# Performance work log

Measured on AMD Instinct MI355X. Metric: run time of the kernel, lower is better.

The kernel has to match this reference:

```python
import jax, jax.numpy as jnp
import numpy as np

B, N, DIN, D, L = 16, 256, 32, 64, 3  # batch, nodes, input feat, emb_dim, num_layer


def setup_inputs() -> dict:
    key = jax.random.key(0)
    ks = jax.random.split(key, 8)
    fea = jax.random.normal(ks[0], (B, N, DIN), jnp.float32)
    # binary dense adjacency (float, as the repo differentiates through it)
    adj = (jax.random.uniform(ks[1], (B, N, N)) < 0.125).astype(jnp.float32)

    def g(k, shape, scale=0.05):
        return jax.random.normal(k, shape, jnp.float32) * scale

    return dict(
        fea=fea, adj=adj,
        enc_W=g(ks[2], (DIN, D)), enc_b=jnp.zeros((D,), jnp.float32),
        bond_W=g(ks[3], (L, D)),            # Linear(1, D, bias=False) per layer
        eps=jnp.zeros((L,), jnp.float32),   # GIN eps per layer
        W1=g(ks[4], (L, D, 2 * D)), b1=jnp.zeros((L, 2 * D), jnp.float32),
        g1=jnp.ones((L, 2 * D), jnp.float32), be1=jnp.zeros((L, 2 * D), jnp.float32),
        W2=g(ks[5], (L, 2 * D, D)), b2=jnp.zeros((L, D), jnp.float32),
        gbn=jnp.ones((L, D), jnp.float32), bbn=jnp.zeros((L, D), jnp.float32),
    )


def _bn(x, gamma, beta, eps=1e-5):
    # BatchNorm1d in training mode: per-channel stats over (batch, nodes)
    m = x.mean((0, 1), keepdims=True)
    v = x.var((0, 1), keepdims=True)
    return (x - m) * jax.lax.rsqrt(v + eps) * gamma + beta


def reference(fea, adj, enc_W, enc_b, bond_W, eps, W1, b1, g1, be1, W2, b2, gbn, bbn):
    x = fea @ enc_W + enc_b                      # [B,N,D] atom_encoder
    adj_ones = jnp.where(adj > 1.0, 1.0, adj)    # clamp multi-bonds to 1
    for l in range(L):
        # GINConv: dense propagate -> message relu(x_j + edge_attr) -> sum over neighbors
        edge = adj[..., None] * bond_W[l]                    # bond_encoder: [B,N,N,D]
        x_j = adj_ones[..., None] * x[:, None, :, :]         # [B,N,N,D] broadcast gather
        agg = jax.nn.relu(x_j + edge).sum(-2)                # [B,N,D] sum-reduce
        h = (1.0 + eps[l]) * x + agg
        # mlp: Linear(D,2D) -> BN -> ReLU -> Linear(2D,D)
        h = _bn(h @ W1[l] + b1[l], g1[l], be1[l])
        h = jax.nn.relu(h) @ W2[l] + b2[l]
        # outer batch norm; ReLU except last layer (drop_ratio=0 -> dropout no-op)
        h = _bn(h, gbn[l], bbn[l])
        x = h if l == L - 1 else jax.nn.relu(h)
    return x  # JK='last'
```

## Files before the change

### kernel.cpp

```cpp
#include <hip/hip_runtime.h>

#define NN 256
#define DIN 32
#define DD 64
#define D2 128
#define RTOT 4096
#define GBD 256
#define RPB 16
#define GBC 512
#define RPC 8
#define AST 32

typedef float f32x4 __attribute__((ext_vector_type(4)));
typedef float f32x2 __attribute__((ext_vector_type(2)));

__device__ __forceinline__ void fma4(f32x4& o, float s, const f32x4 w) {
  o[0] = fmaf(s, w[0], o[0]); o[1] = fmaf(s, w[1], o[1]);
  o[2] = fmaf(s, w[2], o[2]); o[3] = fmaf(s, w[3], o[3]);
}

__global__ __launch_bounds__(256) void enc_kernel(
    const float* __restrict__ fea, const float* __restrict__ W,
    const float* __restrict__ bias, float* __restrict__ x,
    float* __restrict__ accz) {
  if (blockIdx.x < 48) {
#pragma unroll
    for (int i = 0; i < 4; ++i)
      accz[blockIdx.x * 1024 + i * 256 + threadIdx.x] = 0.f;
  }
  int g = blockIdx.x * 256 + threadIdx.x;
  int r = g >> 6, c = g & 63;
  const float* fr = fea + r * DIN;
  float acc = bias[c];
#pragma unroll
  for (int k = 0; k < DIN; ++k) acc = fmaf(fr[k], W[k * DD + c], acc);
  x[g] = acc;
}

__global__ __launch_bounds__(256) void bc_kernel(
    const float* __restrict__ adj, const float* __restrict__ x,
    const float* __restrict__ bondW, const float* __restrict__ epsp,
    const float* __restrict__ W1, const float* __restrict__ b1,
    const float* __restrict__ gbnp, const float* __restrict__ bbnp,
    const float* __restrict__ acc2p,
    int apply_bn,
    float* __restrict__ h1, float* __restrict__ acc1) {
  __shared__ float sY[NN * DD];
  __shared__ float sh[RPC * DD];
  __shared__ float sSB[2 * DD];
  __shared__ float pst[2 * RPC * D2];
  const int tid = threadIdx.x, bid = blockIdx.x;
  const int lane = tid & 63, wv = tid >> 6;
  const int b = bid >> 5;
  const int r0 = (bid & 31) * RPC;

  if (apply_bn && tid < DD) {
    float s = acc2p[tid * AST], q = acc2p[(64 + tid) * AST];
    float mean = s * (1.f / RTOT);
    float var = fmaf(-mean, mean, q * (1.f / RTOT));
    float sc = gbnp[tid] * rsqrtf(var + 1e-5f);
    sSB[tid] = sc;
    sSB[64 + tid] = fmaf(-mean, sc, bbnp[tid]);
  }
  __syncthreads();

  const float* xb = x + (size_t)b * NN * DD;

  float a[2][4];
#pragma unroll
  for (int rr = 0; rr < 2; ++rr) {
    const float* adjr = adj + ((size_t)b * NN + r0 + wv * 2 + rr) * NN + lane;
#pragma unroll
    for (int ck = 0; ck < 4; ++ck) a[rr][ck] = adjr[ck * 64];
  }
  float xo[2];
#pragma unroll
  for (int rr = 0; rr < 2; ++rr)
    xo[rr] = xb[(size_t)(r0 + wv * 2 + rr) * DD + lane];
  f32x4 yv[16];
  {
    const f32x4* xb4 = (const f32x4*)xb;
#pragma unroll
    for (int k = 0; k < 16; ++k) yv[k] = xb4[tid + k * 256];
  }

  unsigned long long m[2][4];
#pragma unroll
  for (int rr = 0; rr < 2; ++rr)
#pragma unroll
    for (int ck = 0; ck < 4; ++ck) m[rr][ck] = __ballot(a[rr][ck] != 0.f);

  {
    const int d0 = (tid & 15) * 4;
    f32x4 bw4 = *(const f32x4*)&bondW[d0];
    f32x4 aS = {0, 0, 0, 0}, aB = {0, 0, 0, 0};
    if (apply_bn) { aS = *(const f32x4*)&sSB[d0]; aB = *(const f32x4*)&sSB[64 + d0]; }
    f32x4* sy4 = (f32x4*)sY;
#pragma unroll
    for (int k = 0; k < 16; ++k) {
      f32x4 v = yv[k];
#pragma unroll
      for (int e = 0; e < 4; ++e) {
        float t = v[e];
        if (apply_bn) t = fmaxf(fmaf(t, aS[e], aB[e]), 0.f);
        v[e] = fmaxf(t + bw4[e], 0.f);
      }
      sy4[tid + k * 256] = v;
    }
  }
  __syncthreads();

  float S = 0.f, Bv = 0.f;
  if (apply_bn) { S = sSB[lane]; Bv = sSB[64 + lane]; }
  float epv = 1.f + epsp[0];
#pragma unroll
  for (int rr = 0; rr < 2; ++rr) {
    float av = 0.f;
#pragma unroll
    for (int ck = 0; ck < 4; ++ck) {
      unsigned long long mm = m[rr][ck];
      const float* yb = sY + ck * 64 * DD + lane;
      while (mm) {
        float v[8]; bool hb[8];
#pragma unroll
        for (int u = 0; u < 8; ++u) {
          bool ok = mm != 0ull;
          int j = ok ? (int)__builtin_ctzll(mm) : 0;
          mm &= mm - 1;
          hb[u] = ok;
          v[u] = yb[j * DD];
        }
#pragma unroll
        for (int u = 0; u < 8; ++u) av += hb[u] ? v[u] : 0.f;
      }
    }
    float xv = xo[rr];
    if (apply_bn) xv = fmaxf(fmaf(xv, S, Bv), 0.f);
    sh[(wv * 2 + rr) * DD + lane] = fmaf(epv, xv, av);
  }
  __syncthreads();

  {
    int row = tid >> 5, c0 = (tid & 31) * 4;
    f32x4 o = *(const f32x4*)&b1[c0];
#pragma unroll 4
    for (int d = 0; d < DD; d += 4) {
      f32x4 hv = *(const f32x4*)&sh[row * DD + d];
      f32x4 w0 = *(const f32x4*)&W1[(d + 0) * D2 + c0];
      f32x4 w1 = *(const f32x4*)&W1[(d + 1) * D2 + c0];
      f32x4 w2 = *(const f32x4*)&W1[(d + 2) * D2 + c0];
      f32x4 w3 = *(const f32x4*)&W1[(d + 3) * D2 + c0];
      fma4(o, hv[0], w0); fma4(o, hv[1], w1); fma4(o, hv[2], w2); fma4(o, hv[3], w3);
    }
    *(f32x4*)&h1[(size_t)(b * NN + r0 + row) * D2 + c0] = o;
    *(f32x4*)&pst[row * D2 + c0] = o;
    *(f32x4*)&pst[RPC * D2 + row * D2 + c0] = o * o;
  }
  __syncthreads();
  if (tid < D2) {
    float s = 0.f, q = 0.f;
#pragma unroll
    for (int g = 0; g < RPC; ++g) {
      s += pst[g * D2 + tid];
      q += pst[RPC * D2 + g * D2 + tid];
    }
    atomicAdd(acc1 + tid * AST, s);
    atomicAdd(acc1 + (128 + tid) * AST, q);
  }
}

__global__ __launch_bounds__(256) void d_kernel(
    const float* __restrict__ h1, const float* __restrict__ W2,
    const float* __restrict__ b2, const float* __restrict__ g1,
    const float* __restrict__ be1, float* __restrict__ h2,
    const float* __restrict__ acc1,
    float* __restrict__ acc2) {
  __shared__ float sW2[D2 * DD];
  __shared__ float sh1[RPB][D2 + 4];
  __shared__ float sS[D2], sB[D2];
  __shared__ float pst[2 * 8 * DD];
  int tid = threadIdx.x, bid = blockIdx.x;

  {
    const f32x4* w4 = (const f32x4*)W2;
    f32x4* s4 = (f32x4*)sW2;
#pragma unroll
    for (int i = 0; i < 8; ++i) s4[tid + i * 256] = w4[tid + i * 256];
  }
  if (tid < D2) {
    float mean = acc1[tid * AST] * (1.f / RTOT);
    float var = fmaf(-mean, mean, acc1[(128 + tid) * AST] * (1.f / RTOT));
    float sc = g1[tid] * rsqrtf(var + 1e-5f);
    sS[tid] = sc;
    sB[tid] = fmaf(-mean, sc, be1[tid]);
  }
  __syncthreads();
  {
    const f32x4* h14 = (const f32x4*)(h1 + (size_t)bid * RPB * D2);
#pragma unroll
    for (int ii = 0; ii < 2; ++ii) {
      int i = tid + ii * 256;
      f32x4 v = h14[i];
      int lr = i >> 5, c = (i & 31) * 4;
      v[0] = fmaxf(fmaf(v[0], sS[c + 0], sB[c + 0]), 0.f);
      v[1] = fmaxf(fmaf(v[1], sS[c + 1], sB[c + 1]), 0.f);
      v[2] = fmaxf(fmaf(v[2], sS[c + 2], sB[c + 2]), 0.f);
      v[3] = fmaxf(fmaf(v[3], sS[c + 3], sB[c + 3]), 0.f);
      *(f32x4*)&sh1[lr][c] = v;
    }
  }
  __syncthreads();

  float* pssum = pst;
  float* pssq  = pst + 8 * DD;
  if (tid < 128) {
    int rg = tid >> 4;
    int c0 = (tid & 15) * 4;
    f32x4 bv = *(const f32x4*)&b2[c0];
    f32x4 o0 = bv, o1 = bv;
    for (int c = 0; c < D2; c += 4) {
      f32x4 s0 = *(const f32x4*)&sh1[rg * 2 + 0][c];
      f32x4 s1 = *(const f32x4*)&sh1[rg * 2 + 1][c];
      f32x4 w0 = *(const f32x4*)&sW2[(c + 0) * DD + c0];
      f32x4 w1 = *(const f32x4*)&sW2[(c + 1) * DD + c0];
      f32x4 w2 = *(const f32x4*)&sW2[(c + 2) * DD + c0];
      f32x4 w3 = *(const f32x4*)&sW2[(c + 3) * DD + c0];
      fma4(o0, s0[0], w0); fma4(o0, s0[1], w1); fma4(o0, s0[2], w2); fma4(o0, s0[3], w3);
      fma4(o1, s1[0], w0); fma4(o1, s1[1], w1); fma4(o1, s1[2], w2); fma4(o1, s1[3], w3);
    }
    size_t gr = (size_t)(bid * RPB + rg * 2) * DD + c0;
    *(f32x4*)&h2[gr] = o0;
    *(f32x4*)&h2[gr + DD] = o1;
    *(f32x4*)&pssum[rg * DD + c0] = o0 + o1;
    *(f32x4*)&pssq[rg * DD + c0] = o0 * o0 + o1 * o1;
  }
  __syncthreads();
  if (tid < DD) {
    float s = 0.f, q = 0.f;
#pragma unroll
    for (int g = 0; g < 8; ++g) { s += pssum[g * DD + tid]; q += pssq[g * DD + tid]; }
    atomicAdd(acc2 + tid * AST, s);
    atomicAdd(acc2 + (64 + tid) * AST, q);
  }
}

__global__ __launch_bounds__(256) void fin_kernel(
    const float* __restrict__ h2, const float* __restrict__ gbn,
    const float* __restrict__ bbn, const float* __restrict__ acc2,
    float* __restrict__ outp) {
  __shared__ float sS2[DD], sB2[DD];
  int tid = threadIdx.x, bid = blockIdx.x;
  if (tid < 64) {
    float mean = acc2[tid * AST] * (1.f / RTOT);
    float var = fmaf(-mean, mean, acc2[(64 + tid) * AST] * (1.f / RTOT));
    float sc = gbn[tid] * rsqrtf(var + 1e-5f);
    sS2[tid] = sc;
    sB2[tid] = fmaf(-mean, sc, bbn[tid]);
  }
  __syncthreads();
#pragma unroll
  for (int k = 0; k < 4; ++k) {
    int idx = bid * 1024 + k * 256 + tid;
    int c = idx & 63;
    outp[idx] = fmaf(h2[idx], sS2[c], sB2[c]);
  }
}

extern "C" void kernel_launch(void* const* d_in, const int* in_sizes, int n_in,
                              void* d_out, int out_size, void* d_ws, size_t ws_size,
                              hipStream_t stream) {
  const float* fea  = (const float*)d_in[0];
  const float* adj  = (const float*)d_in[1];
  const float* encW = (const float*)d_in[2];
  const float* encb = (const float*)d_in[3];
  const float* bondW= (const float*)d_in[4];
  const float* eps  = (const float*)d_in[5];
  const float* W1   = (const float*)d_in[6];
  const float* b1   = (const float*)d_in[7];
  const float* g1   = (const float*)d_in[8];
  const float* be1  = (const float*)d_in[9];
  const float* W2   = (const float*)d_in[10];
  const float* b2   = (const float*)d_in[11];
  const float* gbn  = (const float*)d_in[12];
  const float* bbn  = (const float*)d_in[13];
  float* out = (float*)d_out;
  float* ws  = (float*)d_ws;

  float* x   = ws;
  float* h1  = ws + 262144;
  float* acc = ws + 786432;

  enc_kernel<<<1024, 256, 0, stream>>>(fea, encW, encb, x, acc);
  for (int l = 0; l < 3; ++l) {
    float* accl = acc + (size_t)l * 512 * AST;
    bc_kernel<<<GBC, 256, 0, stream>>>(
        adj, x, bondW + l * DD, eps + l, W1 + l * DD * D2, b1 + l * D2,
        l ? gbn + (l - 1) * DD : gbn, l ? bbn + (l - 1) * DD : bbn,
        l ? acc + (size_t)(l - 1) * 512 * AST + 256 * AST : acc, l > 0 ? 1 : 0,
        h1, accl);
    d_kernel<<<GBD, 256, 0, stream>>>(h1, W2 + l * D2 * DD, b2 + l * DD,
                                      g1 + l * D2, be1 + l * D2, x,
                                      accl, accl + 256 * AST);
  }
  fin_kernel<<<256, 256, 0, stream>>>(x, gbn + 2 * DD, bbn + 2 * DD,
                                      acc + (size_t)2 * 512 * AST + 256 * AST, out);
}
```

Measured before the change: 87.16 us.

## Fuse GIN aggregation and MLP kernels with an in-kernel grid barrier

```diff
diff --git a/kernel.cpp b/kernel.cpp
--- a/kernel.cpp
+++ b/kernel.cpp
@@ -5,11 +5,10 @@
 #define DD 64
 #define D2 128
 #define RTOT 4096
-#define GBD 256
-#define RPB 16
-#define GBC 512
-#define RPC 8
+#define GBL 512
+#define RPL 8
 #define AST 32
+#define DONE_SLOT 500
 
 typedef float f32x4 __attribute__((ext_vector_type(4)));
 typedef float f32x2 __attribute__((ext_vector_type(2)));
@@ -17,6 +16,16 @@
 __device__ __forceinline__ void fma4(f32x4& o, float s, const f32x4 w) {
   o[0] = fmaf(s, w[0], o[0]); o[1] = fmaf(s, w[1], o[1]);
   o[2] = fmaf(s, w[2], o[2]); o[3] = fmaf(s, w[3], o[3]);
+}
+
+__device__ __forceinline__ float cload1(const float* p) {
+  float r;
+  asm volatile("global_load_dword %0, %1, off sc0 sc1\n\ts_waitcnt vmcnt(0)"
+               : "=&v"(r) : "v"(p) : "memory");
+  return r;
+}
+__device__ __forceinline__ void cwait() {
+  asm volatile("s_waitcnt vmcnt(0)" ::: "memory");
 }
 
 __global__ __launch_bounds__(256) void enc_kernel(
@@ -37,22 +46,24 @@
   x[g] = acc;
 }
 
-__global__ __launch_bounds__(256) void bc_kernel(
-    const float* __restrict__ adj, const float* __restrict__ x,
+__global__ __launch_bounds__(256, 2) void layer_kernel(
+    const float* __restrict__ adj, float* __restrict__ x,
     const float* __restrict__ bondW, const float* __restrict__ epsp,
     const float* __restrict__ W1, const float* __restrict__ b1,
+    const float* __restrict__ W2, const float* __restrict__ b2,
+    const float* __restrict__ g1, const float* __restrict__ be1,
     const float* __restrict__ gbnp, const float* __restrict__ bbnp,
     const float* __restrict__ acc2p,
     int apply_bn,
-    float* __restrict__ h1, float* __restrict__ acc1) {
+    float* __restrict__ accl) {
   __shared__ float sY[NN * DD];
-  __shared__ float sh[RPC * DD];
-  __shared__ float sSB[2 * DD];
-  __shared__ float pst[2 * RPC * D2];
+  __shared__ float sh[RPL * DD];
+  __shared__ float sSB[2 * D2];
+  __shared__ float pst[2 * RPL * D2];
   const int tid = threadIdx.x, bid = blockIdx.x;
   const int lane = tid & 63, wv = tid >> 6;
   const int b = bid >> 5;
-  const int r0 = (bid & 31) * RPC;
+  const int r0 = (bid & 31) * RPL;
 
   if (apply_bn && tid < DD) {
     float s = acc2p[tid * AST], q = acc2p[(64 + tid) * AST];
@@ -110,33 +121,35 @@
   }
   __syncthreads();
 
-  float S = 0.f, Bv = 0.f;
-  if (apply_bn) { S = sSB[lane]; Bv = sSB[64 + lane]; }
-  float epv = 1.f + epsp[0];
-#pragma unroll
-  for (int rr = 0; rr < 2; ++rr) {
-    float av = 0.f;
-#pragma unroll
-    for (int ck = 0; ck < 4; ++ck) {
-      unsigned long long mm = m[rr][ck];
-      const float* yb = sY + ck * 64 * DD + lane;
-      while (mm) {
-        float v[8]; bool hb[8];
-#pragma unroll
-        for (int u = 0; u < 8; ++u) {
-          bool ok = mm != 0ull;
-          int j = ok ? (int)__builtin_ctzll(mm) : 0;
-          mm &= mm - 1;
-          hb[u] = ok;
-          v[u] = yb[j * DD];
+  {
+    float S = 0.f, Bv = 0.f;
+    if (apply_bn) { S = sSB[lane]; Bv = sSB[64 + lane]; }
+    float epv = 1.f + epsp[0];
+#pragma unroll
+    for (int rr = 0; rr < 2; ++rr) {
+      float av = 0.f;
+#pragma unroll
+      for (int ck = 0; ck < 4; ++ck) {
+        unsigned long long mm = m[rr][ck];
+        const float* yb = sY + ck * 64 * DD + lane;
+        while (mm) {
+          float v[8]; bool hb[8];
+#pragma unroll
+          for (int u = 0; u < 8; ++u) {
+            bool ok = mm != 0ull;
+            int j = ok ? (int)__builtin_ctzll(mm) : 0;
+            mm &= mm - 1;
+            hb[u] = ok;
+            v[u] = yb[j * DD];
+          }
+#pragma unroll
+          for (int u = 0; u < 8; ++u) av += hb[u] ? v[u] : 0.f;
         }
-#pragma unroll
-        for (int u = 0; u < 8; ++u) av += hb[u] ? v[u] : 0.f;
       }
-    }
-    float xv = xo[rr];
-    if (apply_bn) xv = fmaxf(fmaf(xv, S, Bv), 0.f);
-    sh[(wv * 2 + rr) * DD + lane] = fmaf(epv, xv, av);
+      float xv = xo[rr];
+      if (apply_bn) xv = fmaxf(fmaf(xv, S, Bv), 0.f);
+      sh[(wv * 2 + rr) * DD + lane] = fmaf(epv, xv, av);
+    }
   }
   __syncthreads();
 
@@ -152,95 +165,82 @@
       f32x4 w3 = *(const f32x4*)&W1[(d + 3) * D2 + c0];
       fma4(o, hv[0], w0); fma4(o, hv[1], w1); fma4(o, hv[2], w2); fma4(o, hv[3], w3);
     }
-    *(f32x4*)&h1[(size_t)(b * NN + r0 + row) * D2 + c0] = o;
+    *(f32x4*)&sY[8192 + row * D2 + c0] = o;
     *(f32x4*)&pst[row * D2 + c0] = o;
-    *(f32x4*)&pst[RPC * D2 + row * D2 + c0] = o * o;
+    *(f32x4*)&pst[RPL * D2 + row * D2 + c0] = o * o;
   }
   __syncthreads();
   if (tid < D2) {
     float s = 0.f, q = 0.f;
 #pragma unroll
-    for (int g = 0; g < RPC; ++g) {
+    for (int g = 0; g < RPL; ++g) {
       s += pst[g * D2 + tid];
-      q += pst[RPC * D2 + g * D2 + tid];
-    }
-    atomicAdd(acc1 + tid * AST, s);
-    atomicAdd(acc1 + (128 + tid) * AST, q);
-  }
-}
-
-__global__ __launch_bounds__(256) void d_kernel(
-    const float* __restrict__ h1, const float* __restrict__ W2,
-    const float* __restrict__ b2, const float* __restrict__ g1,
-    const float* __restrict__ be1, float* __restrict__ h2,
-    const float* __restrict__ acc1,
-    float* __restrict__ acc2) {
-  __shared__ float sW2[D2 * DD];
-  __shared__ float sh1[RPB][D2 + 4];
-  __shared__ float sS[D2], sB[D2];
-  __shared__ float pst[2 * 8 * DD];
-  int tid = threadIdx.x, bid = blockIdx.x;
+      q += pst[RPL * D2 + g * D2 + tid];
+    }
+    atomicAdd(accl + tid * AST, s);
+    atomicAdd(accl + (128 + tid) * AST, q);
+  }
 
   {
     const f32x4* w4 = (const f32x4*)W2;
-    f32x4* s4 = (f32x4*)sW2;
-#pragma unroll
-    for (int i = 0; i < 8; ++i) s4[tid + i * 256] = w4[tid + i * 256];
-  }
+#pragma unroll
+    for (int i = 0; i < 8; ++i) ((f32x4*)sY)[tid + i * 256] = w4[tid + i * 256];
+  }
+  cwait();
+  __syncthreads();
+  {
+    unsigned* done = (unsigned*)(accl + DONE_SLOT * AST);
+    if (tid == 0) {
+      __hip_atomic_fetch_add(done, 1u, __ATOMIC_RELAXED, __HIP_MEMORY_SCOPE_AGENT);
+      while (__hip_atomic_load(done, __ATOMIC_RELAXED, __HIP_MEMORY_SCOPE_AGENT) < GBL)
+        __builtin_amdgcn_s_sleep(2);
+    }
+    __syncthreads();
+  }
+
   if (tid < D2) {
-    float mean = acc1[tid * AST] * (1.f / RTOT);
-    float var = fmaf(-mean, mean, acc1[(128 + tid) * AST] * (1.f / RTOT));
+    float s = cload1(accl + tid * AST);
+    float q = cload1(accl + (128 + tid) * AST);
+    float mean = s * (1.f / RTOT);
+    float var = fmaf(-mean, mean, q * (1.f / RTOT));
     float sc = g1[tid] * rsqrtf(var + 1e-5f);
-    sS[tid] = sc;
-    sB[tid] = fmaf(-mean, sc, be1[tid]);
-  }
-  __syncthreads();
-  {
-    const f32x4* h14 = (const f32x4*)(h1 + (size_t)bid * RPB * D2);
-#pragma unroll
-    for (int ii = 0; ii < 2; ++ii) {
-      int i = tid + ii * 256;
-      f32x4 v = h14[i];
-      int lr = i >> 5, c = (i & 31) * 4;
-      v[0] = fmaxf(fmaf(v[0], sS[c + 0], sB[c + 0]), 0.f);
-      v[1] = fmaxf(fmaf(v[1], sS[c + 1], sB[c + 1]), 0.f);
-      v[2] = fmaxf(fmaf(v[2], sS[c + 2], sB[c + 2]), 0.f);
-      v[3] = fmaxf(fmaf(v[3], sS[c + 3], sB[c + 3]), 0.f);
-      *(f32x4*)&sh1[lr][c] = v;
-    }
-  }
-  __syncthreads();
-
-  float* pssum = pst;
-  float* pssq  = pst + 8 * DD;
-  if (tid < 128) {
-    int rg = tid >> 4;
-    int c0 = (tid & 15) * 4;
-    f32x4 bv = *(const f32x4*)&b2[c0];
-    f32x4 o0 = bv, o1 = bv;
-    for (int c = 0; c < D2; c += 4) {
-      f32x4 s0 = *(const f32x4*)&sh1[rg * 2 + 0][c];
-      f32x4 s1 = *(const f32x4*)&sh1[rg * 2 + 1][c];
-      f32x4 w0 = *(const f32x4*)&sW2[(c + 0) * DD + c0];
-      f32x4 w1 = *(const f32x4*)&sW2[(c + 1) * DD + c0];
-      f32x4 w2 = *(const f32x4*)&sW2[(c + 2) * DD + c0];
-      f32x4 w3 = *(const f32x4*)&sW2[(c + 3) * DD + c0];
-      fma4(o0, s0[0], w0); fma4(o0, s0[1], w1); fma4(o0, s0[2], w2); fma4(o0, s0[3], w3);
-      fma4(o1, s1[0], w0); fma4(o1, s1[1], w1); fma4(o1, s1[2], w2); fma4(o1, s1[3], w3);
-    }
-    size_t gr = (size_t)(bid * RPB + rg * 2) * DD + c0;
-    *(f32x4*)&h2[gr] = o0;
-    *(f32x4*)&h2[gr + DD] = o1;
-    *(f32x4*)&pssum[rg * DD + c0] = o0 + o1;
-    *(f32x4*)&pssq[rg * DD + c0] = o0 * o0 + o1 * o1;
+    sSB[tid] = sc;
+    sSB[128 + tid] = fmaf(-mean, sc, be1[tid]);
+  }
+  __syncthreads();
+#pragma unroll
+  for (int ii = 0; ii < 4; ++ii) {
+    int i = tid + ii * 256;
+    int c = i & 127;
+    float v = sY[8192 + i];
+    sY[9216 + i] = fmaxf(fmaf(v, sSB[c], sSB[128 + c]), 0.f);
+  }
+  __syncthreads();
+  {
+    int row = tid >> 5, cp = (tid & 31) * 2;
+    f32x2 o = *(const f32x2*)&b2[cp];
+    const float* hb = sY + 9216 + row * D2;
+#pragma unroll 8
+    for (int c = 0; c < D2; ++c) {
+      float hv = hb[c];
+      f32x2 w = *(const f32x2*)&sY[c * DD + cp];
+      o[0] = fmaf(hv, w[0], o[0]);
+      o[1] = fmaf(hv, w[1], o[1]);
+    }
+    *(f32x2*)&x[(size_t)(b * NN + r0 + row) * DD + cp] = o;
+    *(f32x2*)&pst[row * DD + cp] = o;
+    *(f32x2*)&pst[RPL * DD + row * DD + cp] = o * o;
   }
   __syncthreads();
   if (tid < DD) {
     float s = 0.f, q = 0.f;
 #pragma unroll
-    for (int g = 0; g < 8; ++g) { s += pssum[g * DD + tid]; q += pssq[g * DD + tid]; }
-    atomicAdd(acc2 + tid * AST, s);
-    atomicAdd(acc2 + (64 + tid) * AST, q);
+    for (int g = 0; g < RPL; ++g) {
+      s += pst[g * DD + tid];
+      q += pst[RPL * DD + g * DD + tid];
+    }
+    atomicAdd(accl + (256 + tid) * AST, s);
+    atomicAdd(accl + (320 + tid) * AST, q);
   }
 }
 
@@ -287,20 +287,18 @@
   float* ws  = (float*)d_ws;
 
   float* x   = ws;
-  float* h1  = ws + 262144;
-  float* acc = ws + 786432;
+  float* acc = ws + 262144;
 
   enc_kernel<<<1024, 256, 0, stream>>>(fea, encW, encb, x, acc);
   for (int l = 0; l < 3; ++l) {
     float* accl = acc + (size_t)l * 512 * AST;
-    bc_kernel<<<GBC, 256, 0, stream>>>(
-        adj, x, bondW + l * DD, eps + l, W1 + l * DD * D2, b1 + l * D2,
+    layer_kernel<<<GBL, 256, 0, stream>>>(
+        adj, x, bondW + l * DD, eps + l,
+        W1 + l * DD * D2, b1 + l * D2, W2 + l * D2 * DD, b2 + l * DD,
+        g1 + l * D2, be1 + l * D2,
         l ? gbn + (l - 1) * DD : gbn, l ? bbn + (l - 1) * DD : bbn,
-        l ? acc + (size_t)(l - 1) * 512 * AST + 256 * AST : acc, l > 0 ? 1 : 0,
-        h1, accl);
-    d_kernel<<<GBD, 256, 0, stream>>>(h1, W2 + l * D2 * DD, b2 + l * DD,
-                                      g1 + l * D2, be1 + l * D2, x,
-                                      accl, accl + 256 * AST);
+        l ? acc + (size_t)(l - 1) * 512 * AST + 256 * AST : acc,
+        l > 0 ? 1 : 0, accl);
   }
   fin_kernel<<<256, 256, 0, stream>>>(x, gbn + 2 * DD, bbn + 2 * DD,
                                       acc + (size_t)2 * 512 * AST + 256 * AST, out);
```

After: 194.3 us. +122.9%, slower.
